# Performance work log

Measured on AMD Instinct MI355X. Metric: run time of the kernel, lower is better.

## Reference

```python
import jax, jax.numpy as jnp
import numpy as np

B, T, VOCAB = 32, 512, 1024
D, H, O, L = 256, 256, 1024, 2


def setup_inputs() -> dict:
    key = jax.random.key(0)
    ks = jax.random.split(key, 7)
    s = 0.02  # keep activations numerically tame across the recurrence
    return {
        "x": jax.random.normal(ks[0], (B, T, VOCAB), dtype=jnp.float32),
        "hidden_states": jax.random.normal(ks[1], (L, H), dtype=jnp.float32),
        "W_emb": jax.random.normal(ks[2], (D, VOCAB), dtype=jnp.float32) * s,
        "W": jax.random.normal(ks[3], (L, H, D), dtype=jnp.float32) * s,
        "U": jax.random.normal(ks[4], (L, H, H), dtype=jnp.float32) * s,
        "V": jax.random.normal(ks[5], (L, D, H), dtype=jnp.float32) * s,
        "W_out": jax.random.normal(ks[6], (O, D), dtype=jnp.float32) * s,
        "stack_length": L,
    }


def reference(x, hidden_states, W_emb, W, U, V, W_out, stack_length):
    # Embedding: Linear(V->D, no bias) => x @ W_emb.T
    inp = jnp.einsum('btv,dv->btd', x, W_emb)  # [B,T,D]
    b = x.shape[0]
    for l in range(stack_length):
        Wl, Ul, Vl = W[l], U[l], V[l]
        h0 = jnp.broadcast_to(hidden_states[l], (b, Ul.shape[0]))  # [B,H]

        def step(h, xt):
            # h_new = W_l x_t + U_l h ; out_t = V_l h_new
            h_new = xt @ Wl.T + h @ Ul.T
            return h_new, h_new @ Vl.T

        _, outs = jax.lax.scan(step, h0, jnp.swapaxes(inp, 0, 1))  # outs: [T,B,D]
        inp = jnp.swapaxes(outs, 0, 1)  # [B,T,D]
    logits = inp @ W_out.T  # [B,T,O]
    # Original applies softmax over dim=1 (the sequence dimension) — keep faithful.
    return jax.nn.softmax(logits, axis=1)
```

## Files before the change

kernel.cpp:

```cpp
#include <hip/hip_runtime.h>
#include <stdint.h>
#include <stddef.h>

typedef short s8v __attribute__((ext_vector_type(8)));
typedef short s4v __attribute__((ext_vector_type(4)));
typedef float f4v __attribute__((ext_vector_type(4)));

#define DEV static __device__ __forceinline__


DEV short f2b(float f) {
  union { float f; uint32_t u; } v; v.f = f;
  uint32_t u = v.u;
  uint32_t r = (u + 0x7fffu + ((u >> 16) & 1u)) >> 16;
  return (short)(uint16_t)r;
}
DEV float b2f(short h) {
  union { uint32_t u; float f; } v; v.u = ((uint32_t)(uint16_t)h) << 16;
  return v.f;
}

DEV void gl_lds16(const void* g, void* l) {
  __builtin_amdgcn_global_load_lds(
      (__attribute__((address_space(1))) void*)(uintptr_t)(g),
      (__attribute__((address_space(3))) void*)(l), 16, 0, 0);
}

DEV void lds_barrier() {
  __builtin_amdgcn_sched_barrier(0);
  asm volatile("s_waitcnt lgkmcnt(0)" ::: "memory");
  __builtin_amdgcn_s_barrier();
  __builtin_amdgcn_sched_barrier(0);
}

DEV int hoff(int s, int k) {
  return ((k >> 5) << 9) + (((k >> 3) & 3) << 7) + (s << 3) + (k & 7);
}

DEV void wgemm_body(const float* __restrict__ Af, const float* __restrict__ Bsrc,
                    short* __restrict__ C, int lda, int ldbs, int ldc,
                    int m0, int n0, int tid, short* As, float* Bf) {
  const int w = tid >> 6, lane = tid & 63, quad = lane >> 4, sid = lane & 15;
  const int wm = (w >> 1) * 64, wn = (w & 1) * 64;

  f4v acc[4][4];
#pragma unroll
  for (int i = 0; i < 4; ++i)
#pragma unroll
    for (int j = 0; j < 4; ++j) acc[i][j] = (f4v){0.f, 0.f, 0.f, 0.f};

  for (int k0 = 0; k0 < 256; k0 += 64) {
#pragma unroll
    for (int q = 0; q < 8; ++q) {
      int lin = q * 256 + tid;
      int kr = lin >> 5, nc = (lin & 31) << 2;
      gl_lds16(Bsrc + (size_t)(k0 + kr) * ldbs + n0 + nc, &Bf[lin << 2]);
    }
#pragma unroll
    for (int q = 0; q < 4; ++q) {
      int lin = q * 256 + tid;
      int row = lin >> 3, kc = (lin & 7) << 3;
      const float* ap = Af + (size_t)(m0 + row) * lda + k0 + kc;
      float4 v0 = *(const float4*)ap;
      float4 v1 = *(const float4*)(ap + 4);
      s8v p;
      p[0] = f2b(v0.x); p[1] = f2b(v0.y); p[2] = f2b(v0.z); p[3] = f2b(v0.w);
      p[4] = f2b(v1.x); p[5] = f2b(v1.y); p[6] = f2b(v1.z); p[7] = f2b(v1.w);
      *(s8v*)&As[row * 72 + kc] = p;
    }
    __syncthreads();
#pragma unroll
    for (int kb = 0; kb < 2; ++kb) {
      s8v af[4], bf[4];
#pragma unroll
      for (int mt = 0; mt < 4; ++mt)
        af[mt] = *(const s8v*)&As[(wm + 16 * mt + sid) * 72 + kb * 32 + quad * 8];
#pragma unroll
      for (int nt = 0; nt < 4; ++nt) {
        s8v b;
#pragma unroll
        for (int j = 0; j < 8; ++j)
          b[j] = f2b(Bf[(kb * 32 + quad * 8 + j) * 128 + wn + 16 * nt + sid]);
        bf[nt] = b;
      }
#pragma unroll
      for (int mt = 0; mt < 4; ++mt)
#pragma unroll
        for (int nt = 0; nt < 4; ++nt)
          acc[mt][nt] = __builtin_amdgcn_mfma_f32_16x16x32_bf16(af[mt], bf[nt], acc[mt][nt], 0, 0, 0);
    }
    __syncthreads();
  }
#pragma unroll
  for (int mt = 0; mt < 4; ++mt)
#pragma unroll
    for (int r = 0; r < 4; ++r) {
      int gm = m0 + wm + 16 * mt + 4 * quad + r;
      size_t ro = (size_t)gm * ldc;
#pragma unroll
      for (int nt = 0; nt < 4; ++nt)
        C[ro + n0 + wn + 16 * nt + sid] = f2b(acc[mt][nt][r]);
    }
}

__global__ __launch_bounds__(256) void wgemm(const float* __restrict__ wemb,
                                             const float* __restrict__ wf,
                                             const float* __restrict__ vfp,
                                             const float* __restrict__ wout,
                                             const float* __restrict__ ufp,
                                             short* __restrict__ a0,
                                             short* __restrict__ a1,
                                             short* __restrict__ a2,
                                             short* __restrict__ ub) {
  __shared__ __align__(16) short As[128 * 72];
  __shared__ __align__(16) float Bf[64 * 128];
  const int blk = blockIdx.x, tid = threadIdx.x;
  if (blk < 16) {
    wgemm_body(wf, wemb, a0, 256, 1024, 1024,
               (blk >> 3) * 128, (blk & 7) * 128, tid, As, Bf);
  } else if (blk < 20) {
    int b = blk - 16;
    wgemm_body(wf + 65536, vfp, a1, 256, 256, 256,
               (b >> 1) * 128, (b & 1) * 128, tid, As, Bf);
  } else if (blk < 36) {
    int b = blk - 20;
    wgemm_body(wout, vfp + 65536, a2, 256, 256, 256,
               (b >> 1) * 128, (b & 1) * 128, tid, As, Bf);
  } else {
    int b = blk - 36;
    const float* src = ufp + (size_t)b * 32768;
    short* dst = ub + (size_t)b * 32768;
#pragma unroll 4
    for (int i = tid; i < 8192; i += 256) {
      float4 v = ((const float4*)src)[i];
      s4v q; q.x = f2b(v.x); q.y = f2b(v.y); q.z = f2b(v.z); q.w = f2b(v.w);
      ((s4v*)dst)[i] = q;
    }
  }
}

__global__ __launch_bounds__(256, 2) void gemm_x(const float* __restrict__ Xf,
                                                 const short* __restrict__ Bw,
                                                 short* __restrict__ C) {
  __shared__ __align__(16) short As[2][32 * 72];
  __shared__ __align__(16) short Bs[2][256 * 64];
  const int tid = threadIdx.x;
  const int w = tid >> 6, lane = tid & 63, quad = lane >> 4, sid = lane & 15;
  const int g = blockIdx.x >> 8, tp = blockIdx.x & 255;
  const int wn = w * 64;

  const int arow = tid >> 3, akc = (tid & 7) << 3;
  const int am = (g * 16 + (arow & 15)) * 512 + 2 * tp + (arow >> 4);
  const float* aptr = &Xf[(size_t)am * 1024 + akc];

#define GX_STAGE(buf, k0)                                                     \
  {                                                                           \
    _Pragma("unroll")                                                         \
    for (int q = 0; q < 8; ++q) {                                             \
      int lin = q * 256 + tid;                                                \
      gl_lds16(Bw + (size_t)(lin >> 3) * 1024 + (k0) + ((lin & 7) << 3),      \
               &Bs[buf][lin << 3]);                                           \
    }                                                                         \
    const float* ap = aptr + (k0);                                            \
    float4 v0 = *(const float4*)ap;                                           \
    float4 v1 = *(const float4*)(ap + 4);                                     \
    s8v p;                                                                    \
    p[0] = f2b(v0.x); p[1] = f2b(v0.y); p[2] = f2b(v0.z); p[3] = f2b(v0.w);   \
    p[4] = f2b(v1.x); p[5] = f2b(v1.y); p[6] = f2b(v1.z); p[7] = f2b(v1.w);   \
    *(s8v*)&As[buf][arow * 72 + akc] = p;                                     \
  }

  f4v acc[2][4];
#pragma unroll
  for (int i = 0; i < 2; ++i)
#pragma unroll
    for (int j = 0; j < 4; ++j) acc[i][j] = (f4v){0.f, 0.f, 0.f, 0.f};

  GX_STAGE(0, 0);
  __syncthreads();
  for (int it = 0; it < 16; ++it) {
    const int cur = it & 1;
    if (it < 15) GX_STAGE(cur ^ 1, (it + 1) * 64);
#pragma unroll
    for (int kb = 0; kb < 2; ++kb) {
      s8v af[2], bf[4];
#pragma unroll
      for (int mt = 0; mt < 2; ++mt)
        af[mt] = *(const s8v*)&As[cur][(16 * mt + sid) * 72 + kb * 32 + quad * 8];
#pragma unroll
      for (int nt = 0; nt < 4; ++nt)
        bf[nt] = *(const s8v*)&Bs[cur][(wn + 16 * nt + sid) * 64 + kb * 32 + quad * 8];
#pragma unroll
      for (int mt = 0; mt < 2; ++mt)
#pragma unroll
        for (int nt = 0; nt < 4; ++nt)
          acc[mt][nt] = __builtin_amdgcn_mfma_f32_16x16x32_bf16(af[mt], bf[nt], acc[mt][nt], 0, 0, 0);
    }
    __syncthreads();
  }
#undef GX_STAGE

  short* Ls = &Bs[0][0];
#pragma unroll
  for (int mt = 0; mt < 2; ++mt)
#pragma unroll
    for (int nt = 0; nt < 4; ++nt) {
      int n = wn + 16 * nt + sid;
#pragma unroll
      for (int r = 0; r < 4; ++r)
        Ls[(16 * mt + 4 * quad + r) * 264 + n] = f2b(acc[mt][nt][r]);
    }
  __syncthreads();
  {
    const size_t obase = (size_t)((g << 9) + 2 * tp) * 4096;
#pragma unroll
    for (int h = 0; h < 2; ++h) {
      int q = h * 256 + tid;
      int tl = q >> 8, q16 = q & 255;
      int ch = q16 >> 3, qq = q16 & 7;
      s4v lo = *(const s4v*)&Ls[(tl * 16 + 2 * qq) * 264 + ch * 4];
      s4v hi = *(const s4v*)&Ls[(tl * 16 + 2 * qq + 1) * 264 + ch * 4];
      s8v v;
      v[0] = lo.x; v[1] = lo.y; v[2] = lo.z; v[3] = lo.w;
      v[4] = hi.x; v[5] = hi.y; v[6] = hi.z; v[7] = hi.w;
      *(s8v*)&C[obase + (size_t)tl * 4096 + q16 * 8] = v;
    }
  }
}

__global__ __launch_bounds__(256, 1) void scan_fuse(const short* __restrict__ Ub,
                                                    const short* __restrict__ A1b,
                                                    const short* __restrict__ XcIn,
                                                    short* __restrict__ XcOut,
                                                    const float* __restrict__ hinit) {
  constexpr int CL = 4, WU = 12, NC = 128;
  __shared__ __align__(16) short hT[2][4096];
  const int tid = threadIdx.x;
  const int w = tid >> 6, lane = tid & 63, quad = lane >> 4, sid = lane & 15;
  const int c = blockIdx.x & (NC - 1);
  const int g = blockIdx.x >> 7;
  const int laneoff = quad * 64 + sid * 4;

  s8v uf[4][8], vf[4][8];
#pragma unroll
  for (int mt = 0; mt < 4; ++mt)
#pragma unroll
    for (int kb = 0; kb < 8; ++kb) {
      int i = 64 * w + 16 * mt + sid;
      int k = 32 * kb + quad * 8;
      uf[mt][kb] = *(const s8v*)&Ub[i * 256 + k];
      vf[mt][kb] = *(const s8v*)&A1b[i * 256 + k];
    }

  const int t0 = (c * CL <= WU) ? 0 : c * CL - WU;
  const int t1 = (c + 1) * CL;

  for (int idx = tid; idx < 4096; idx += 256) {
    int s = idx >> 8, i = idx & 255;
    hT[0][hoff(s, i)] = (t0 == 0) ? f2b(hinit[i]) : (short)0;
  }
  __syncthreads();

  s4v xcn[4];
  {
    const size_t xb = (size_t)((g << 9) + t0) * 4096 + 1024 * w + laneoff;
#pragma unroll
    for (int mt = 0; mt < 4; ++mt)
      xcn[mt] = *(const s4v*)&XcIn[xb + 256 * mt];
  }

  int pr = 0;
  for (int t = t0; t <= t1; ++t) {
    s8v bf[8];
#pragma unroll
    for (int kb = 0; kb < 8; ++kb)
      bf[kb] = *(const s8v*)&hT[pr][kb * 512 + quad * 128 + sid * 8];
    const bool doh = (t < t1);
    s4v xcc[4];
    if (doh) {
#pragma unroll
      for (int mt = 0; mt < 4; ++mt) xcc[mt] = xcn[mt];
    }
    if (t + 1 < t1) {
      const size_t xb = (size_t)((g << 9) + t + 1) * 4096 + 1024 * w + laneoff;
#pragma unroll
      for (int mt = 0; mt < 4; ++mt)
        xcn[mt] = *(const s4v*)&XcIn[xb + 256 * mt];
    }

    if (t > c * CL) {
      f4v ax[4];
#pragma unroll
      for (int mt = 0; mt < 4; ++mt) ax[mt] = (f4v){0.f, 0.f, 0.f, 0.f};
#pragma unroll
      for (int kb = 0; kb < 8; ++kb)
#pragma unroll
        for (int mt = 0; mt < 4; ++mt)
          ax[mt] = __builtin_amdgcn_mfma_f32_16x16x32_bf16(vf[mt][kb], bf[kb], ax[mt], 0, 0, 0);
      const size_t ob = (size_t)((g << 9) + (t - 1)) * 4096 + 1024 * w + laneoff;
#pragma unroll
      for (int mt = 0; mt < 4; ++mt) {
        s4v p; p.x = f2b(ax[mt].x); p.y = f2b(ax[mt].y);
        p.z = f2b(ax[mt].z); p.w = f2b(ax[mt].w);
        *(s4v*)&XcOut[ob + 256 * mt] = p;
      }
    }

    if (doh) {
      f4v acc[4];
#pragma unroll
      for (int mt = 0; mt < 4; ++mt) acc[mt] = (f4v){0.f, 0.f, 0.f, 0.f};
#pragma unroll
      for (int kb = 0; kb < 8; ++kb)
#pragma unroll
        for (int mt = 0; mt < 4; ++mt)
          acc[mt] = __builtin_amdgcn_mfma_f32_16x16x32_bf16(uf[mt][kb], bf[kb], acc[mt], 0, 0, 0);
#pragma unroll
      for (int mt = 0; mt < 4; ++mt) {
        int k0 = 64 * w + 16 * mt + 4 * quad;
        f4v v = acc[mt];
        v.x += b2f(xcc[mt].x); v.y += b2f(xcc[mt].y);
        v.z += b2f(xcc[mt].z); v.w += b2f(xcc[mt].w);
        s4v p; p.x = f2b(v.x); p.y = f2b(v.y); p.z = f2b(v.z); p.w = f2b(v.w);
        *(s4v*)&hT[pr ^ 1][hoff(sid, k0)] = p;
      }
    }
    pr ^= 1;
    lds_barrier();
  }
}

__global__ __launch_bounds__(256, 2) void scan_rnn(const short* __restrict__ Ub,
                                                   const short* __restrict__ XcT,
                                                   short* __restrict__ hbuf,
                                                   const float* __restrict__ hinit) {
  constexpr int CL = 2, WU = 12, NC = 256;
  __shared__ __align__(16) short hT[2][4096];
  const int tid = threadIdx.x;
  const int w = tid >> 6, lane = tid & 63, quad = lane >> 4, sid = lane & 15;
  const int c = blockIdx.x & (NC - 1);
  const int g = blockIdx.x >> 8;
  const int laneoff = quad * 64 + sid * 4;

  s8v uf[4][8];
#pragma unroll
  for (int mt = 0; mt < 4; ++mt)
#pragma unroll
    for (int kb = 0; kb < 8; ++kb) {
      int i = 64 * w + 16 * mt + sid;
      int k = 32 * kb + quad * 8;
      uf[mt][kb] = *(const s8v*)&Ub[i * 256 + k];
    }

  const int t0 = (c * CL <= WU) ? 0 : c * CL - WU;
  const int t1 = (c + 1) * CL;

  for (int idx = tid; idx < 4096; idx += 256) {
    int s = idx >> 8, i = idx & 255;
    hT[0][hoff(s, i)] = (t0 == 0) ? f2b(hinit[i]) : (short)0;
  }
  __syncthreads();

  s4v xcn[4];
  {
    const size_t xb = (size_t)((g << 9) + t0) * 4096 + 1024 * w + laneoff;
#pragma unroll
    for (int mt = 0; mt < 4; ++mt)
      xcn[mt] = *(const s4v*)&XcT[xb + 256 * mt];
  }

  int pr = 0;
  for (int t = t0; t < t1; ++t) {
    s8v bf[8];
#pragma unroll
    for (int kb = 0; kb < 8; ++kb)
      bf[kb] = *(const s8v*)&hT[pr][kb * 512 + quad * 128 + sid * 8];
    s4v xcc[4];
#pragma unroll
    for (int mt = 0; mt < 4; ++mt) xcc[mt] = xcn[mt];
    if (t + 1 < t1) {
      const size_t xb = (size_t)((g << 9) + t + 1) * 4096 + 1024 * w + laneoff;
#pragma unroll
      for (int mt = 0; mt < 4; ++mt)
        xcn[mt] = *(const s4v*)&XcT[xb + 256 * mt];
    }

    f4v acc[4];
#pragma unroll
    for (int mt = 0; mt < 4; ++mt) acc[mt] = (f4v){0.f, 0.f, 0.f, 0.f};
#pragma unroll
    for (int kb = 0; kb < 8; ++kb)
#pragma unroll
      for (int mt = 0; mt < 4; ++mt)
        acc[mt] = __builtin_amdgcn_mfma_f32_16x16x32_bf16(uf[mt][kb], bf[kb], acc[mt], 0, 0, 0);

    const bool emit = (t >= c * CL);
    const size_t xbase = ((size_t)((g << 9) + t) * 16 + sid) * 256;
#pragma unroll
    for (int mt = 0; mt < 4; ++mt) {
      int k0 = 64 * w + 16 * mt + 4 * quad;
      f4v v = acc[mt];
      v.x += b2f(xcc[mt].x); v.y += b2f(xcc[mt].y);
      v.z += b2f(xcc[mt].z); v.w += b2f(xcc[mt].w);
      s4v p; p.x = f2b(v.x); p.y = f2b(v.y); p.z = f2b(v.z); p.w = f2b(v.w);
      *(s4v*)&hT[pr ^ 1][hoff(sid, k0)] = p;
      if (emit) *(s4v*)&hbuf[xbase + k0] = p;
    }
    pr ^= 1;
    lds_barrier();
  }
}

__global__ __launch_bounds__(256, 2) void gemm_logsm(const short* __restrict__ A,
                                                     const short* __restrict__ Bw,
                                                     float* __restrict__ out) {
  __shared__ __align__(16) short As[512 * 40];
  __shared__ __align__(16) short Bs[64 * 32];
  __shared__ float2 red[4][64];
  const int tid = threadIdx.x;
  const int w = tid >> 6, lane = tid & 63, quad = lane >> 4, sid = lane & 15;
  const int b = blockIdx.x & 31, ot = blockIdx.x >> 5;
  const int g = b >> 4, si = b & 15;

  f4v acc[8][4];
#pragma unroll
  for (int i = 0; i < 8; ++i)
#pragma unroll
    for (int j = 0; j < 4; ++j) acc[i][j] = (f4v){0.f, 0.f, 0.f, 0.f};

  const int at = (tid * 4 + 1024 * 0) >> 2;
  (void)at;
  const int brow = tid & 63, bkch = tid >> 6;
  const short* bptr = Bw + (size_t)(ot * 64 + brow) * 256 + bkch * 8;

  s8v va[8], vb;
#pragma unroll
  for (int q = 0; q < 8; ++q) {
    int lin = q * 256 + tid;
    int t = lin >> 2, kch = lin & 3;
    size_t ar = ((size_t)(g * 512 + t) * 16 + si) * 256;
    va[q] = *(const s8v*)(A + ar + kch * 8);
  }
  vb = *(const s8v*)bptr;

  for (int it = 0; it < 8; ++it) {
#pragma unroll
    for (int q = 0; q < 8; ++q) {
      int lin = q * 256 + tid;
      int t = lin >> 2, kch = lin & 3;
      *(s8v*)&As[t * 40 + kch * 8] = va[q];
    }
    *(s8v*)&Bs[tid << 3] = vb;
    __syncthreads();
    if (it < 7) {
      int k0n = (it + 1) * 32;
#pragma unroll
      for (int q = 0; q < 8; ++q) {
        int lin = q * 256 + tid;
        int t = lin >> 2, kch = lin & 3;
        size_t ar = ((size_t)(g * 512 + t) * 16 + si) * 256;
        va[q] = *(const s8v*)(A + ar + k0n + kch * 8);
      }
      vb = *(const s8v*)(bptr + k0n);
    }
    s8v bf[4];
#pragma unroll
    for (int nt = 0; nt < 4; ++nt)
      bf[nt] = *(const s8v*)&Bs[(quad * 64 + 16 * nt + sid) * 8];
#pragma unroll
    for (int mt = 0; mt < 8; ++mt) {
      s8v af = *(const s8v*)&As[(128 * w + 16 * mt + sid) * 40 + quad * 8];
#pragma unroll
      for (int nt = 0; nt < 4; ++nt)
        acc[mt][nt] = __builtin_amdgcn_mfma_f32_16x16x32_bf16(af, bf[nt], acc[mt][nt], 0, 0, 0);
    }
    __syncthreads();
  }

  float Mv[4], Iv[4];
#pragma unroll
  for (int nt = 0; nt < 4; ++nt) {
    float m = -3.0e38f;
#pragma unroll
    for (int mt = 0; mt < 8; ++mt)
#pragma unroll
      for (int r = 0; r < 4; ++r) m = fmaxf(m, acc[mt][nt][r]);
    float sum = 0.f;
#pragma unroll
    for (int mt = 0; mt < 8; ++mt)
#pragma unroll
      for (int r = 0; r < 4; ++r) sum += __expf(acc[mt][nt][r] - m);
#pragma unroll
    for (int d = 16; d < 64; d <<= 1) {
      float om = __shfl_xor(m, d, 64);
      float os = __shfl_xor(sum, d, 64);
      float nm = fmaxf(m, om);
      sum = sum * __expf(m - nm) + os * __expf(om - nm);
      m = nm;
    }
    if (quad == 0) red[w][16 * nt + sid] = (float2){m, sum};
  }
  __syncthreads();
#pragma unroll
  for (int nt = 0; nt < 4; ++nt) {
    float M = -3.0e38f, S = 0.f;
#pragma unroll
    for (int ww = 0; ww < 4; ++ww) {
      float2 r2 = red[ww][16 * nt + sid];
      float nm = fmaxf(M, r2.x);
      S = S * __expf(M - nm) + r2.y * __expf(r2.x - nm);
      M = nm;
    }
    Mv[nt] = M;
    Iv[nt] = 1.0f / S;
  }

  const size_t cbase = (size_t)b * 524288 + ot * 64 + sid;
#pragma unroll
  for (int nt = 0; nt < 4; ++nt) {
    const size_t cb = cbase + 16 * nt;
#pragma unroll
    for (int mt = 0; mt < 8; ++mt)
#pragma unroll
      for (int r = 0; r < 4; ++r) {
        int t = 128 * w + 16 * mt + 4 * quad + r;
        out[cb + (size_t)t * 1024] = __expf(acc[mt][nt][r] - Mv[nt]) * Iv[nt];
      }
  }
}

extern "C" void kernel_launch(void* const* d_in, const int* in_sizes, int n_in,
                              void* d_out, int out_size, void* d_ws, size_t ws_size,
                              hipStream_t stream) {
  (void)in_sizes; (void)n_in; (void)out_size; (void)ws_size;
  const float* xf   = (const float*)d_in[0];
  const float* hs   = (const float*)d_in[1];
  const float* wemb = (const float*)d_in[2];
  const float* wf   = (const float*)d_in[3];
  const float* ufp  = (const float*)d_in[4];
  const float* vfp  = (const float*)d_in[5];
  const float* wout = (const float*)d_in[6];

  char* ws = (char*)d_ws;
  short* hbuf = (short*)(ws);
  short* xcT0 = (short*)(ws + 8388608);
  short* xcT1 = (short*)(ws + 16777216);
  short* a0   = (short*)(ws + 25165824);
  short* a1   = (short*)(ws + 25690112);
  short* a2   = (short*)(ws + 25821184);
  short* ub   = (short*)(ws + 26345472);

  wgemm<<<40, 256, 0, stream>>>(wemb, wf, vfp, wout, ufp, a0, a1, a2, ub);

  gemm_x<<<512, 256, 0, stream>>>(xf, a0, xcT0);

  scan_fuse<<<256, 256, 0, stream>>>(ub, a1, xcT0, xcT1, hs);

  scan_rnn<<<512, 256, 0, stream>>>(ub + 65536, xcT1, hbuf, hs + 256);

  gemm_logsm<<<512, 256, 0, stream>>>(hbuf, a2, (float*)d_out);
}
```

Measured before the change: 228.7 us.

## Split scan_fuse into two warp groups for recurrence and output projection

scan_fuse now launches 512 threads per block. Warps 0-3 compute the recurrent U·h update into LDS, and warps 4-7 concurrently compute the layer-1 output projection (A1·h) and write it to global memory. Each warp now holds only one weight matrix in registers instead of two, which halves register pressure and lets the two MFMA chains run on separate waves within the same timestep. The trade-off is a barrier shared across 8 waves, and the projection group sits idle whenever the U group dominates the critical path.

```diff
diff --git a/kernel.cpp b/kernel.cpp
--- a/kernel.cpp
+++ b/kernel.cpp
@@ -228,7 +228,7 @@
   }
 }
 
-__global__ __launch_bounds__(256, 1) void scan_fuse(const short* __restrict__ Ub,
+__global__ __launch_bounds__(512, 2) void scan_fuse(const short* __restrict__ Ub,
                                                     const short* __restrict__ A1b,
                                                     const short* __restrict__ XcIn,
                                                     short* __restrict__ XcOut,
@@ -236,34 +236,35 @@
   constexpr int CL = 4, WU = 12, NC = 128;
   __shared__ __align__(16) short hT[2][4096];
   const int tid = threadIdx.x;
-  const int w = tid >> 6, lane = tid & 63, quad = lane >> 4, sid = lane & 15;
+  const int w2 = tid >> 6, lane = tid & 63, quad = lane >> 4, sid = lane & 15;
+  const int grp = w2 >> 2, wl = w2 & 3;
   const int c = blockIdx.x & (NC - 1);
   const int g = blockIdx.x >> 7;
   const int laneoff = quad * 64 + sid * 4;
 
-  s8v uf[4][8], vf[4][8];
+  s8v wfr[4][8];
+  const short* Wsrc = grp ? A1b : Ub;
 #pragma unroll
   for (int mt = 0; mt < 4; ++mt)
 #pragma unroll
     for (int kb = 0; kb < 8; ++kb) {
-      int i = 64 * w + 16 * mt + sid;
+      int i = 64 * wl + 16 * mt + sid;
       int k = 32 * kb + quad * 8;
-      uf[mt][kb] = *(const s8v*)&Ub[i * 256 + k];
-      vf[mt][kb] = *(const s8v*)&A1b[i * 256 + k];
+      wfr[mt][kb] = *(const s8v*)&Wsrc[i * 256 + k];
     }
 
   const int t0 = (c * CL <= WU) ? 0 : c * CL - WU;
   const int t1 = (c + 1) * CL;
 
-  for (int idx = tid; idx < 4096; idx += 256) {
+  for (int idx = tid; idx < 4096; idx += 512) {
     int s = idx >> 8, i = idx & 255;
     hT[0][hoff(s, i)] = (t0 == 0) ? f2b(hinit[i]) : (short)0;
   }
   __syncthreads();
 
-  s4v xcn[4];
-  {
-    const size_t xb = (size_t)((g << 9) + t0) * 4096 + 1024 * w + laneoff;
+  s4v xcn[4] = {};
+  if (grp == 0) {
+    const size_t xb = (size_t)((g << 9) + t0) * 4096 + 1024 * wl + laneoff;
 #pragma unroll
     for (int mt = 0; mt < 4; ++mt)
       xcn[mt] = *(const s4v*)&XcIn[xb + 256 * mt];
@@ -275,54 +276,56 @@
 #pragma unroll
     for (int kb = 0; kb < 8; ++kb)
       bf[kb] = *(const s8v*)&hT[pr][kb * 512 + quad * 128 + sid * 8];
-    const bool doh = (t < t1);
-    s4v xcc[4];
-    if (doh) {
-#pragma unroll
-      for (int mt = 0; mt < 4; ++mt) xcc[mt] = xcn[mt];
-    }
-    if (t + 1 < t1) {
-      const size_t xb = (size_t)((g << 9) + t + 1) * 4096 + 1024 * w + laneoff;
-#pragma unroll
-      for (int mt = 0; mt < 4; ++mt)
-        xcn[mt] = *(const s4v*)&XcIn[xb + 256 * mt];
-    }
-
-    if (t > c * CL) {
-      f4v ax[4];
-#pragma unroll
-      for (int mt = 0; mt < 4; ++mt) ax[mt] = (f4v){0.f, 0.f, 0.f, 0.f};
-#pragma unroll
-      for (int kb = 0; kb < 8; ++kb)
+
+    if (grp == 0) {
+      const bool doh = (t < t1);
+      s4v xcc[4];
+      if (doh) {
+#pragma unroll
+        for (int mt = 0; mt < 4; ++mt) xcc[mt] = xcn[mt];
+      }
+      if (t + 1 < t1) {
+        const size_t xb = (size_t)((g << 9) + t + 1) * 4096 + 1024 * wl + laneoff;
 #pragma unroll
         for (int mt = 0; mt < 4; ++mt)
-          ax[mt] = __builtin_amdgcn_mfma_f32_16x16x32_bf16(vf[mt][kb], bf[kb], ax[mt], 0, 0, 0);
-      const size_t ob = (size_t)((g << 9) + (t - 1)) * 4096 + 1024 * w + laneoff;
-#pragma unroll
-      for (int mt = 0; mt < 4; ++mt) {
-        s4v p; p.x = f2b(ax[mt].x); p.y = f2b(ax[mt].y);
-        p.z = f2b(ax[mt].z); p.w = f2b(ax[mt].w);
-        *(s4v*)&XcOut[ob + 256 * mt] = p;
-      }
-    }
-
-    if (doh) {
-      f4v acc[4];
-#pragma unroll
-      for (int mt = 0; mt < 4; ++mt) acc[mt] = (f4v){0.f, 0.f, 0.f, 0.f};
-#pragma unroll
-      for (int kb = 0; kb < 8; ++kb)
-#pragma unroll
-        for (int mt = 0; mt < 4; ++mt)
-          acc[mt] = __builtin_amdgcn_mfma_f32_16x16x32_bf16(uf[mt][kb], bf[kb], acc[mt], 0, 0, 0);
-#pragma unroll
-      for (int mt = 0; mt < 4; ++mt) {
-        int k0 = 64 * w + 16 * mt + 4 * quad;
-        f4v v = acc[mt];
-        v.x += b2f(xcc[mt].x); v.y += b2f(xcc[mt].y);
-        v.z += b2f(xcc[mt].z); v.w += b2f(xcc[mt].w);
-        s4v p; p.x = f2b(v.x); p.y = f2b(v.y); p.z = f2b(v.z); p.w = f2b(v.w);
-        *(s4v*)&hT[pr ^ 1][hoff(sid, k0)] = p;
+          xcn[mt] = *(const s4v*)&XcIn[xb + 256 * mt];
+      }
+      if (doh) {
+        f4v acc[4];
+#pragma unroll
+        for (int mt = 0; mt < 4; ++mt) acc[mt] = (f4v){0.f, 0.f, 0.f, 0.f};
+#pragma unroll
+        for (int kb = 0; kb < 8; ++kb)
+#pragma unroll
+          for (int mt = 0; mt < 4; ++mt)
+            acc[mt] = __builtin_amdgcn_mfma_f32_16x16x32_bf16(wfr[mt][kb], bf[kb], acc[mt], 0, 0, 0);
+#pragma unroll
+        for (int mt = 0; mt < 4; ++mt) {
+          int k0 = 64 * wl + 16 * mt + 4 * quad;
+          f4v v = acc[mt];
+          v.x += b2f(xcc[mt].x); v.y += b2f(xcc[mt].y);
+          v.z += b2f(xcc[mt].z); v.w += b2f(xcc[mt].w);
+          s4v p; p.x = f2b(v.x); p.y = f2b(v.y); p.z = f2b(v.z); p.w = f2b(v.w);
+          *(s4v*)&hT[pr ^ 1][hoff(sid, k0)] = p;
+        }
+      }
+    } else {
+      if (t > c * CL) {
+        f4v ax[4];
+#pragma unroll
+        for (int mt = 0; mt < 4; ++mt) ax[mt] = (f4v){0.f, 0.f, 0.f, 0.f};
+#pragma unroll
+        for (int kb = 0; kb < 8; ++kb)
+#pragma unroll
+          for (int mt = 0; mt < 4; ++mt)
+            ax[mt] = __builtin_amdgcn_mfma_f32_16x16x32_bf16(wfr[mt][kb], bf[kb], ax[mt], 0, 0, 0);
+        const size_t ob = (size_t)((g << 9) + (t - 1)) * 4096 + 1024 * wl + laneoff;
+#pragma unroll
+        for (int mt = 0; mt < 4; ++mt) {
+          s4v p; p.x = f2b(ax[mt].x); p.y = f2b(ax[mt].y);
+          p.z = f2b(ax[mt].z); p.w = f2b(ax[mt].w);
+          *(s4v*)&XcOut[ob + 256 * mt] = p;
+        }
       }
     }
     pr ^= 1;
@@ -428,8 +431,6 @@
 #pragma unroll
     for (int j = 0; j < 4; ++j) acc[i][j] = (f4v){0.f, 0.f, 0.f, 0.f};
 
-  const int at = (tid * 4 + 1024 * 0) >> 2;
-  (void)at;
   const int brow = tid & 63, bkch = tid >> 6;
   const short* bptr = Bw + (size_t)(ot * 64 + brow) * 256 + bkch * 8;
 
@@ -554,7 +555,7 @@
 
   gemm_x<<<512, 256, 0, stream>>>(xf, a0, xcT0);
 
-  scan_fuse<<<256, 256, 0, stream>>>(ub, a1, xcT0, xcT1, hs);
+  scan_fuse<<<256, 512, 0, stream>>>(ub, a1, xcT0, xcT1, hs);
 
   scan_rnn<<<512, 256, 0, stream>>>(ub + 65536, xcT1, hbuf, hs + 256);
 
```

After: 227.3 us. No clear change (-0.6%).
